# Performance work log

Measured on AMD Instinct MI355X. Metric: run time of the kernel, lower is better.

Reference implementation:

```python
import jax, jax.numpy as jnp
import numpy as np

EPS_S = 1e-06
EPS_SUM = 1e-08
EPS_LOG = 1e-08


def gram_eigh_svd(h_flat):
    """h_flat: (B, N, k) float32 -> (S: (B,k) desc, Vh: (B,k,k)).
    SVD of h_flat via eigendecomposition of the k x k gram matrix."""
    G = jnp.einsum('bnk,bnm->bkm', h_flat, h_flat)  # (B, k, k)
    evals, evecs = jnp.linalg.eigh(G)               # ascending eigenvalues
    S = jnp.sqrt(jnp.clip(evals, 0.0, None))[:, ::-1]          # descending
    Vh = jnp.swapaxes(evecs[:, :, ::-1], -2, -1)                # rows = right singular vectors
    return S, Vh


def extract_features(S, Vh):
    """(B,k), (B,k,k) -> (B, 2k+2)."""
    S_safe = jnp.clip(S, EPS_S, None)
    s_norm = S_safe / (jnp.sum(S_safe, axis=-1, keepdims=True) + EPS_SUM)
    vh_diag = jnp.diagonal(Vh, axis1=-2, axis2=-1)                       # (B, k)
    vh_offdiag = jnp.clip(
        jnp.sum(Vh * Vh, axis=(-2, -1)) - jnp.sum(vh_diag * vh_diag, axis=-1),
        0.0, None)[:, None]                                              # (B, 1)
    s_ent = -jnp.sum(s_norm * jnp.log(jnp.clip(s_norm, EPS_LOG, None)),
                     axis=-1, keepdims=True)                             # (B, 1)
    out = jnp.concatenate([s_norm, vh_diag, vh_offdiag, s_ent], axis=-1)
    return jnp.where(jnp.isfinite(out), out, jnp.zeros_like(out))


def setup_inputs() -> dict:
    key = jax.random.key(0)
    k1, k2 = jax.random.split(key)
    B, C, H, W = 64, 512, 64, 64
    k = 24
    x = jax.random.normal(k1, (B, C, H, W), dtype=jnp.float32)
    w_proj = jax.random.normal(k2, (k, C), dtype=jnp.float32) * (1.0 / np.sqrt(C))
    ema_s = jnp.ones((k,), dtype=jnp.float32)
    return {"x": x, "w_proj": w_proj, "ema_s": ema_s}


def reference(x, w_proj, ema_s):
    B, C, H, W = x.shape
    k = w_proj.shape[0]
    # 1x1 conv == per-pixel matmul; go straight to (B, H*W, k)
    h_flat = jnp.einsum('bchw,kc->bhwk', x, w_proj).reshape(B, H * W, k)
    # torch path runs eigh under no_grad / fp32
    S, Vh = gram_eigh_svd(jax.lax.stop_gradient(h_flat.astype(jnp.float32)))
    S = jnp.clip(S, EPS_S, None)
    S = jnp.where(jnp.isfinite(S), S, jnp.ones_like(S))
    Vh = jnp.where(jnp.isfinite(Vh), Vh, jnp.zeros_like(Vh))
    features = extract_features(S, Vh)
    novelty = S - ema_s[None, :]
    return (S, Vh, features, novelty)
```

## Files before the change

### kernel.cpp

```cpp
#include <hip/hip_runtime.h>
#include <math.h>


#define N24 24
#define ZS 25

__global__ __launch_bounds__(256) void proj_gram_kernel(
    const float* __restrict__ x, const float* __restrict__ w,
    double* __restrict__ partial)
{
    const int b   = blockIdx.x >> 2;
    const int q   = blockIdx.x & 3;
    const int tid = threadIdx.x;
    const int n0  = (q << 10) | (tid << 2);
    __shared__ __align__(16) float smem[24 * 512];
    float* wl = smem;
    for (int i2 = tid; i2 < 24 * 512; i2 += 256) wl[i2] = w[i2];
    __syncthreads();

    const float* xb = x + ((size_t)b << 21) + n0;
    float h[4][24];
#pragma unroll
    for (int j = 0; j < 4; ++j)
#pragma unroll
        for (int k = 0; k < 24; ++k) h[j][k] = 0.f;

    float4 cA[8];
#pragma unroll
    for (int t = 0; t < 8; ++t)
        cA[t] = *reinterpret_cast<const float4*>(xb + ((size_t)t << 12));

    for (int c = 0; c < 512; c += 8) {
        float4 cB[8];
        if (c + 8 < 512) {
#pragma unroll
            for (int t = 0; t < 8; ++t)
                cB[t] = *reinterpret_cast<const float4*>(xb + ((size_t)(c + 8 + t) << 12));
        }
#pragma unroll
        for (int sub = 0; sub < 2; ++sub) {
            const float4 a0 = cA[sub * 4 + 0];
            const float4 a1 = cA[sub * 4 + 1];
            const float4 a2 = cA[sub * 4 + 2];
            const float4 a3 = cA[sub * 4 + 3];
            const int cc = c + sub * 4;
#pragma unroll
            for (int k = 0; k < 24; ++k) {
                const float4 wv = *reinterpret_cast<const float4*>(&wl[k * 512 + cc]);
                h[0][k] += wv.x * a0.x + wv.y * a1.x + wv.z * a2.x + wv.w * a3.x;
                h[1][k] += wv.x * a0.y + wv.y * a1.y + wv.z * a2.y + wv.w * a3.y;
                h[2][k] += wv.x * a0.z + wv.y * a1.z + wv.z * a2.z + wv.w * a3.z;
                h[3][k] += wv.x * a0.w + wv.y * a1.w + wv.z * a2.w + wv.w * a3.w;
            }
        }
#pragma unroll
        for (int t = 0; t < 8; ++t) cA[t] = cB[t];
    }
    __syncthreads();

    float* hl = smem;
    const int s_own = tid >> 6, l64 = tid & 63;
    for (int s2 = 0; s2 < 4; ++s2) {
        if (s_own == s2) {
#pragma unroll
            for (int j = 0; j < 4; ++j)
#pragma unroll
                for (int k = 0; k < 24; ++k)
                    hl[((l64 << 2) + j) * 24 + k] = h[j][k];
        }
        __syncthreads();
        for (int p = tid; p < 300; p += 256) {
            int k = 0, pp = p;
            while (pp >= 24 - k) { pp -= 24 - k; ++k; }
            int m = k + pp;
            double acc = 0.0;
            for (int i2 = 0; i2 < 256; ++i2)
                acc += (double)hl[i2 * 24 + k] * (double)hl[i2 * 24 + m];
            partial[((size_t)(b * 16 + (q << 2) + s2)) * 300 + p] = acc;
        }
        __syncthreads();
    }
}

__global__ __launch_bounds__(320) void gram_reduce_kernel(
    const double* __restrict__ partial, float* __restrict__ G)
{
    const int b = blockIdx.x;
    const int p = threadIdx.x;
    if (p >= 300) return;
    int k = 0, pp = p;
    while (pp >= 24 - k) { pp -= 24 - k; ++k; }
    int m = k + pp;
    double acc = 0.0;
    for (int t = 0; t < 16; ++t)
        acc += partial[((size_t)(b * 16 + t)) * 300 + p];
    float v = (float)acc;
    G[b * 576 + k * 24 + m] = v;
    G[b * 576 + m * 24 + k] = v;
}

__device__ __forceinline__ float rlf(float v, int l) {
    return __int_as_float(__builtin_amdgcn_readlane(__float_as_int(v), l));
}

__device__ __forceinline__ float lapy2f(float xx, float yy) {
#pragma clang fp contract(off)
    float xa = fabsf(xx), ya = fabsf(yy);
    float w = fmaxf(xa, ya), z = fminf(xa, ya);
    float q = z / w;
    float res = w * sqrtf(1.f + q * q);
    return (z == 0.f) ? w : res;
}

__device__ __forceinline__ void slartg_(float f, float g, float& c, float& s, float& r) {
#pragma clang fp contract(off)
    float f1 = fabsf(f), g1 = fabsf(g);
    const float rtmin_ = 0x1p-63f;
    const float rtmax_ = 1.8446743e+19f;
    bool inr = (f1 > rtmin_) && (f1 < rtmax_) && (g1 > rtmin_) && (g1 < rtmax_);
    if (__builtin_expect(!inr && f != 0.f && g != 0.f, 0)) {
        float u = fminf(3.4028235e+38f, fmaxf(0x1p-126f, fmaxf(f1, g1)));
        float fs = f / u, gs = g / u;
        float d = sqrtf(fs * fs + gs * gs);
        float p = 1.f / d;
        c = fabsf(fs) * p;
        s = gs * copysignf(p, f);
        r = copysignf(d, f) * u;
    } else {
        float d = sqrtf(f * f + g * g);
        float p = 1.f / d;
        float cN = f1 * p;
        float sN = g * copysignf(p, f);
        float rN = copysignf(d, f);
        bool gz = (g == 0.f), fz = (f == 0.f);
        c = gz ? 1.f : (fz ? 0.f : cN);
        s = gz ? 0.f : (fz ? copysignf(1.f, g) : sN);
        r = gz ? f   : (fz ? g1 : rN);
    }
}

__device__ __forceinline__ void slaev2_(float a, float b, float cc,
                                        float& rt1, float& rt2, float& cs1, float& sn1) {
#pragma clang fp contract(off)
    float sm = a + cc, df = a - cc, adf = fabsf(df);
    float tb = b + b, ab = fabsf(tb);
    float acmx, acmn;
    if (fabsf(a) > fabsf(cc)) { acmx = a; acmn = cc; } else { acmx = cc; acmn = a; }
    float rt;
    if (adf > ab)      { float q = ab / adf; rt = adf * sqrtf(1.f + q * q); }
    else if (adf < ab) { float q = adf / ab; rt = ab * sqrtf(1.f + q * q); }
    else               rt = ab * sqrtf(2.f);
    int sgn1;
    if (sm < 0.f)      { rt1 = 0.5f * (sm - rt); sgn1 = -1; rt2 = (acmx / rt1) * acmn - (b / rt1) * b; }
    else if (sm > 0.f) { rt1 = 0.5f * (sm + rt); sgn1 =  1; rt2 = (acmx / rt1) * acmn - (b / rt1) * b; }
    else               { rt1 = 0.5f * rt; rt2 = -0.5f * rt; sgn1 = 1; }
    float cs; int sgn2;
    if (df >= 0.f) { cs = df + rt; sgn2 = 1; } else { cs = df - rt; sgn2 = -1; }
    float acs = fabsf(cs);
    if (acs > ab) { float ct = -tb / cs; sn1 = 1.f / sqrtf(1.f + ct * ct); cs1 = ct * sn1; }
    else {
        if (ab == 0.f) { cs1 = 1.f; sn1 = 0.f; }
        else { float tn = -cs / tb; cs1 = 1.f / sqrtf(1.f + tn * tn); sn1 = tn * cs1; }
    }
    if (sgn1 == sgn2) { float tn = cs1; cs1 = -sn1; sn1 = tn; }
}

#define RD(j)   rlf(dr, (j) - 1)
#define RE(j)   rlf(er, (j) - 1)
#define WD(j,v) { float _v = (v); int _j = (j) - 1; dr = (lane == _j) ? _v : dr; }
#define WE(j,v) { float _v = (v); int _j = (j) - 1; er = (lane == _j) ? _v : er; }

__global__ __launch_bounds__(64) void eigh_feat_kernel(
    const float* __restrict__ G, const float* __restrict__ ema,
    float* __restrict__ out)
{
#pragma clang fp contract(off)
    const int b = blockIdx.x;
    const int lane = threadIdx.x;
    const int n = N24;

    __shared__ float A[N24 * N24];
    __shared__ float Zl[N24 * ZS];
    __shared__ float dl[N24 + 1], el[N24 + 1], tau[N24 + 1];
    __shared__ float hv[N24], hw[N24];
    __shared__ float Sarr[N24], snorm[N24];

    for (int idx = lane; idx < n * n; idx += 64) A[idx] = G[(size_t)b * n * n + idx];
    __syncthreads();

    for (int i = 0; i < n - 1; ++i) {
        const int mlen = n - 1 - i;
        float alpha = A[(i + 1) + N24 * i];
        float ss = 0.f;
        for (int r = i + 2; r < n; ++r) { float t = A[r + N24 * i]; ss += t * t; }
        float xnorm = sqrtf(ss);
        if (xnorm == 0.f) {
            if (lane == 0) { tau[i + 1] = 0.f; el[i + 1] = alpha; dl[i + 1] = A[i + N24 * i]; }
            __syncthreads();
            continue;
        }
        float beta = -copysignf(lapy2f(alpha, xnorm), alpha);
        float taui = (beta - alpha) / beta;
        float scal = 1.f / (alpha - beta);
        if (lane == 0) { tau[i + 1] = taui; el[i + 1] = beta; }
        __syncthreads();
        if (lane >= i + 2 && lane < n) A[lane + N24 * i] *= scal;
        __syncthreads();
        if (lane < mlen) hv[lane] = (lane == 0) ? 1.f : A[(i + 1 + lane) + N24 * i];
        __syncthreads();
        if (lane < mlen) {
            float acc = 0.f;
            int gr = i + 1 + lane;
            for (int c2 = 0; c2 < mlen; ++c2) {
                int gc = i + 1 + c2;
                float av = (gr >= gc) ? A[gr + N24 * gc] : A[gc + N24 * gr];
                acc += av * hv[c2];
            }
            hw[lane] = taui * acc;
        }
        __syncthreads();
        float dot = 0.f;
        for (int r2 = 0; r2 < mlen; ++r2) dot += hw[r2] * hv[r2];
        float alpha2 = -0.5f * taui * dot;
        __syncthreads();
        if (lane < mlen) hw[lane] += alpha2 * hv[lane];
        __syncthreads();
        if (lane < mlen) {
            for (int c2 = 0; c2 <= lane; ++c2)
                A[(i + 1 + lane) + N24 * (i + 1 + c2)] -= hv[lane] * hw[c2] + hw[lane] * hv[c2];
        }
        __syncthreads();
        if (lane == 0) dl[i + 1] = A[i + N24 * i];
        __syncthreads();
    }
    if (lane == 0) dl[n] = A[(n - 1) + N24 * (n - 1)];
    __syncthreads();

    for (int idx = lane; idx < N24 * ZS; idx += 64) Zl[idx] = 0.f;
    __syncthreads();
    if (lane < n) Zl[lane + ZS * lane] = 1.f;
    __syncthreads();

    float dr = (lane < 24) ? dl[lane + 1] : 0.f;
    float er = (lane < 23) ? el[lane + 1] : 0.f;
    float wcr = 0.f, wsr = 0.f;

    {
        const float eps_    = 0x1p-24f;
        const float eps2_   = 0x1p-48f;
        const float safmin_ = 0x1p-126f;
        const float ssfmax_ = 3.0744573e+18f;
        const float ssfmin_ = 0x1p-15f;
        const int nmaxit = n * 30;
        int jtot = 0, l1 = 1;
        int l = 0, lsv = 0, lend = 0, lendsv = 0, mb = 0, iscale = 0;
        float anorm = 0.f, p = 0.f, g = 0.f, r_ = 0.f, c_ = 0.f, s_ = 0.f, f_ = 0.f, b_ = 0.f;
        float rt1 = 0.f, rt2 = 0.f, cc = 0.f, sn = 0.f;
        int m_ = 0, i_ = 0, j_ = 0;

L10:
        if (l1 > n) goto L160;
        if (l1 > 1) WE(l1 - 1, 0.f);
        {
            float dnx = __shfl_down(dr, 1, 64);
            float ae = fabsf(er);
            bool inr = (lane >= l1 - 1) && (lane <= n - 2);
            bool t0 = inr && (ae == 0.f);
            bool t1 = inr && (ae <= (sqrtf(fabsf(dr)) * sqrtf(fabsf(dnx))) * eps_);
            unsigned long long msk0 = __ballot(t0);
            unsigned long long mskc = msk0 | __ballot(t1);
            if (mskc) {
                int bit = __builtin_ctzll(mskc);
                m_ = bit + 1;
                bool wasz = (msk0 >> bit) & 1ull;
                if (!wasz) WE(m_, 0.f);
            } else m_ = n;
        }
        l = l1; lsv = l; lend = m_; lendsv = lend; l1 = m_ + 1;
        if (lend == l) goto L10;

        {
            bool ind = (lane >= l - 1) && (lane <= lend - 1);
            bool ine = (lane >= l - 1) && (lane <= lend - 2);
            float v = fmaxf(ind ? fabsf(dr) : 0.f, ine ? fabsf(er) : 0.f);
            for (int off = 32; off; off >>= 1) v = fmaxf(v, __shfl_xor(v, off, 64));
            anorm = v;
        }
        iscale = 0;
        if (anorm == 0.f) goto L10;
        if (anorm > ssfmax_) {
            iscale = 1;
            float mul = ssfmax_ / anorm;
            if (lane + 1 >= l && lane + 1 <= lend) dr *= mul;
            if (lane + 1 >= l && lane + 1 <= lend - 1) er *= mul;
        } else if (anorm < ssfmin_) {
            iscale = 2;
            float mul = ssfmin_ / anorm;
            if (lane + 1 >= l && lane + 1 <= lend) dr *= mul;
            if (lane + 1 >= l && lane + 1 <= lend - 1) er *= mul;
        }
        if (fabsf(RD(lend)) < fabsf(RD(l))) { lend = lsv; l = lendsv; }

        if (lend > l) {
L40:
            if (l != lend) {
                float dnx = __shfl_down(dr, 1, 64);
                bool inr = (lane >= l - 1) && (lane <= lend - 2);
                bool t = inr && (er * er <= (eps2_ * fabsf(dr)) * fabsf(dnx) + safmin_);
                unsigned long long msk = __ballot(t);
                m_ = msk ? (__builtin_ctzll(msk) + 1) : lend;
            } else m_ = lend;
            if (m_ < lend) WE(m_, 0.f);
            mb = m_;
            p = RD(l);
            if (mb == l) goto L80;
            if (mb == l + 1) {
                slaev2_(RD(l), RE(l), RD(l + 1), rt1, rt2, cc, sn);
                if (lane < n) {
                    float z1 = Zl[lane + ZS * l];
                    float z0 = Zl[lane + ZS * (l - 1)];
                    Zl[lane + ZS * l]       = cc * z1 - sn * z0;
                    Zl[lane + ZS * (l - 1)] = sn * z1 + cc * z0;
                }
                WD(l, rt1); WD(l + 1, rt2); WE(l, 0.f);
                l = l + 2;
                if (l <= lend) goto L40;
                goto L140;
            }
            if (jtot == nmaxit) goto L140;
            jtot = jtot + 1;
            {
                float dmb = RD(mb);
                g = (RD(l + 1) - p) / (2.f * RE(l));
                r_ = lapy2f(g, 1.f);
                g = dmb - p + (RE(l) / (g + copysignf(r_, g)));
                s_ = 1.f; c_ = 1.f; p = 0.f;
                float dcar = dmb;
                for (i_ = mb - 1; i_ >= l; --i_) {
                    float ei = RE(i_);
                    float di = RD(i_);
                    f_ = s_ * ei;
                    b_ = c_ * ei;
                    slartg_(g, f_, c_, s_, r_);
                    er = ((i_ != mb - 1) && (lane == i_)) ? r_ : er;
                    g = dcar - p;
                    r_ = (di - g) * s_ + 2.f * c_ * b_;
                    p = s_ * r_;
                    dr = (lane == i_) ? (g + p) : dr;
                    g = c_ * r_ - b_;
                    bool w3 = (lane == i_ - 1);
                    wcr = w3 ? c_ : wcr;
                    wsr = w3 ? -s_ : wsr;
                    dcar = di;
                }
                if (lane < n) {
                    float carry = Zl[lane + ZS * (mb - 1)];
                    for (j_ = mb - 1; j_ >= l; --j_) {
                        float cj = rlf(wcr, j_ - 1), sj = rlf(wsr, j_ - 1);
                        float prev = Zl[lane + ZS * (j_ - 1)];
                        Zl[lane + ZS * j_] = cj * carry - sj * prev;
                        carry = sj * carry + cj * prev;
                    }
                    Zl[lane + ZS * (l - 1)] = carry;
                }
                WD(l, dcar - p);
                WE(l, g);
            }
            goto L40;
L80:
            WD(l, p);
            l = l + 1;
            if (l <= lend) goto L40;
            goto L140;
        } else {
L90:
            if (l != lend) {
                float epu = __shfl_up(er, 1, 64);
                float dup = __shfl_up(dr, 1, 64);
                bool inr = (lane >= lend) && (lane <= l - 1);
                bool t = inr && (epu * epu <= (eps2_ * fabsf(dr)) * fabsf(dup) + safmin_);
                unsigned long long msk = __ballot(t);
                if (msk) {
                    m_ = 63 - __builtin_clzll(msk) + 1;
                } else m_ = lend;
            } else m_ = lend;
            if (m_ > lend) WE(m_ - 1, 0.f);
            mb = m_;
            p = RD(l);
            if (mb == l) goto L130;
            if (mb == l - 1) {
                slaev2_(RD(l - 1), RE(l - 1), RD(l), rt1, rt2, cc, sn);
                if (lane < n) {
                    float z1 = Zl[lane + ZS * (l - 1)];
                    float z0 = Zl[lane + ZS * (l - 2)];
                    Zl[lane + ZS * (l - 1)] = cc * z1 - sn * z0;
                    Zl[lane + ZS * (l - 2)] = sn * z1 + cc * z0;
                }
                WD(l - 1, rt1); WD(l, rt2); WE(l - 1, 0.f);
                l = l - 2;
                if (l >= lend) goto L90;
                goto L140;
            }
            if (jtot == nmaxit) goto L140;
            jtot = jtot + 1;
            {
                float dmb = RD(mb);
                g = (RD(l - 1) - p) / (2.f * RE(l - 1));
                r_ = lapy2f(g, 1.f);
                g = dmb - p + (RE(l - 1) / (g + copysignf(r_, g)));
                s_ = 1.f; c_ = 1.f; p = 0.f;
                float dcar = dmb;
                for (i_ = mb; i_ <= l - 1; ++i_) {
                    float ei = RE(i_);
                    float dnx = RD(i_ + 1);
                    f_ = s_ * ei;
                    b_ = c_ * ei;
                    slartg_(g, f_, c_, s_, r_);
                    er = ((i_ != mb) && (lane == i_ - 2)) ? r_ : er;
                    g = dcar - p;
                    r_ = (dnx - g) * s_ + 2.f * c_ * b_;
                    p = s_ * r_;
                    dr = (lane == i_ - 1) ? (g + p) : dr;
                    g = c_ * r_ - b_;
                    bool w3 = (lane == i_ - 1);
                    wcr = w3 ? c_ : wcr;
                    wsr = w3 ? s_ : wsr;
                    dcar = dnx;
                }
                if (lane < n) {
                    float carryPrev = Zl[lane + ZS * (mb - 1)];
                    for (j_ = mb; j_ <= l - 1; ++j_) {
                        float cj = rlf(wcr, j_ - 1), sj = rlf(wsr, j_ - 1);
                        float t = Zl[lane + ZS * j_];
                        Zl[lane + ZS * (j_ - 1)] = sj * t + cj * carryPrev;
                        carryPrev = cj * t - sj * carryPrev;
                    }
                    Zl[lane + ZS * (l - 1)] = carryPrev;
                }
                WD(l, dcar - p);
                WE(l - 1, g);
            }
            goto L90;
L130:
            WD(l, p);
            l = l - 1;
            if (l >= lend) goto L90;
            goto L140;
        }
L140:
        if (iscale == 1) {
            float mul = anorm / ssfmax_;
            if (lane + 1 >= lsv && lane + 1 <= lendsv) dr *= mul;
            if (lane + 1 >= lsv && lane + 1 <= lendsv - 1) er *= mul;
        } else if (iscale == 2) {
            float mul = anorm / ssfmin_;
            if (lane + 1 >= lsv && lane + 1 <= lendsv) dr *= mul;
            if (lane + 1 >= lsv && lane + 1 <= lendsv - 1) er *= mul;
        }
        if (jtot < nmaxit) goto L10;
        goto L160;

L160:
        for (int ii = 2; ii <= n; ++ii) {
            int ia = ii - 1;
            float val = (lane >= ii - 2 && lane <= n - 1) ? dr : __builtin_inff();
            int idx = lane + 1;
            for (int off = 32; off; off >>= 1) {
                float v2 = __shfl_xor(val, off, 64);
                int   i2 = __shfl_xor(idx, off, 64);
                bool take = (v2 < val) || ((v2 == val) && (i2 < idx));
                val = take ? v2 : val;
                idx = take ? i2 : idx;
            }
            int ka = idx;
            float pp = val;
            if (ka != ia) {
                float dia = RD(ia);
                WD(ka, dia);
                WD(ia, pp);
                if (lane < n) {
                    float t = Zl[lane + ZS * (ia - 1)];
                    Zl[lane + ZS * (ia - 1)] = Zl[lane + ZS * (ka - 1)];
                    Zl[lane + ZS * (ka - 1)] = t;
                }
            }
        }
    }

    if (lane < 24) dl[lane + 1] = dr;
    __syncthreads();

    for (int i = n - 2; i >= 0; --i) {
        float taui = tau[i + 1];
        if (taui != 0.f && lane < n) {
            int j = lane;
            float w_ = Zl[(i + 1) + ZS * j];
            for (int r = i + 2; r < n; ++r) w_ += A[r + N24 * i] * Zl[r + ZS * j];
            Zl[(i + 1) + ZS * j] -= taui * w_;
            for (int r = i + 2; r < n; ++r) Zl[r + ZS * j] -= taui * (A[r + N24 * i] * w_);
        }
        __syncthreads();
    }

    const int S_OFF = 0, VH_OFF = 1536, F_OFF = 38400, NOV_OFF = 41600;
    if (lane < n) {
        float ev = dl[n - lane];
        float s0 = sqrtf(fmaxf(ev, 0.f));
        s0 = fmaxf(s0, 1e-6f);
        if (!isfinite(s0)) s0 = 1.f;
        Sarr[lane] = s0;
    }
    __syncthreads();
    if (lane < n) {
        out[S_OFF + b * 24 + lane] = Sarr[lane];
        out[NOV_OFF + b * 24 + lane] = Sarr[lane] - ema[lane];
    }
    for (int idx = lane; idx < 576; idx += 64) {
        int j = idx / 24, i2 = idx % 24;
        float vv = Zl[i2 + ZS * (23 - j)];
        if (!isfinite(vv)) vv = 0.f;
        out[VH_OFF + b * 576 + idx] = vv;
    }
    float sum_ = 0.f;
    for (int j2 = 0; j2 < n; ++j2) sum_ += Sarr[j2];
    float denom = sum_ + 1e-8f;
    if (lane < n) snorm[lane] = Sarr[lane] / denom;
    __syncthreads();
    float ent = 0.f;
    for (int j2 = 0; j2 < n; ++j2) {
        float sn2 = snorm[j2];
        ent -= sn2 * logf(fmaxf(sn2, 1e-8f));
    }
    float sumsq = 0.f, diagsq = 0.f;
    for (int j2 = 0; j2 < n; ++j2)
        for (int i2 = 0; i2 < n; ++i2) { float z = Zl[i2 + ZS * j2]; sumsq += z * z; }
    for (int j2 = 0; j2 < n; ++j2) { float dv = Zl[j2 + ZS * (23 - j2)]; diagsq += dv * dv; }
    float offd = fmaxf(sumsq - diagsq, 0.f);
    if (lane < n) {
        float v0 = snorm[lane]; if (!isfinite(v0)) v0 = 0.f;
        out[F_OFF + b * 50 + lane] = v0;
        float dv = Zl[lane + ZS * (23 - lane)]; if (!isfinite(dv)) dv = 0.f;
        out[F_OFF + b * 50 + 24 + lane] = dv;
    }
    if (lane == 0) {
        if (!isfinite(offd)) offd = 0.f;
        if (!isfinite(ent)) ent = 0.f;
        out[F_OFF + b * 50 + 48] = offd;
        out[F_OFF + b * 50 + 49] = ent;
    }
}

extern "C" void kernel_launch(void* const* d_in, const int* in_sizes, int n_in,
                              void* d_out, int out_size, void* d_ws, size_t ws_size,
                              hipStream_t stream)
{
    const float* x   = (const float*)d_in[0];
    const float* w   = (const float*)d_in[1];
    const float* ema = (const float*)d_in[2];
    float* out = (float*)d_out;

    double* partial = (double*)d_ws;
    float* G = (float*)((char*)d_ws + (size_t)1024 * 300 * sizeof(double));

    hipLaunchKernelGGL(proj_gram_kernel, dim3(256), dim3(256), 0, stream, x, w, partial);
    hipLaunchKernelGGL(gram_reduce_kernel, dim3(64), dim3(320), 0, stream, partial, G);
    hipLaunchKernelGGL(eigh_feat_kernel, dim3(64), dim3(64), 0, stream, G, ema, out);
}
```

Before: 507.7 us.

## Double projection grid to 512 blocks and split eigh into three kernels

```diff
diff --git a/kernel.cpp b/kernel.cpp
--- a/kernel.cpp
+++ b/kernel.cpp
@@ -4,53 +4,52 @@
 
 #define N24 24
 #define ZS 25
+#define HS 25
 
 __global__ __launch_bounds__(256) void proj_gram_kernel(
     const float* __restrict__ x, const float* __restrict__ w,
     double* __restrict__ partial)
 {
-    const int b   = blockIdx.x >> 2;
-    const int q   = blockIdx.x & 3;
+    const int b   = blockIdx.x >> 3;
+    const int q8  = blockIdx.x & 7;
     const int tid = threadIdx.x;
-    const int n0  = (q << 10) | (tid << 2);
-    __shared__ __align__(16) float smem[24 * 512];
+    const int n0  = (q8 << 9) | (tid << 1);
+    __shared__ __align__(16) float smem[512 * HS];
     float* wl = smem;
     for (int i2 = tid; i2 < 24 * 512; i2 += 256) wl[i2] = w[i2];
     __syncthreads();
 
     const float* xb = x + ((size_t)b << 21) + n0;
-    float h[4][24];
-#pragma unroll
-    for (int j = 0; j < 4; ++j)
+    float h[2][24];
+#pragma unroll
+    for (int j = 0; j < 2; ++j)
 #pragma unroll
         for (int k = 0; k < 24; ++k) h[j][k] = 0.f;
 
-    float4 cA[8];
+    float2 cA[8];
 #pragma unroll
     for (int t = 0; t < 8; ++t)
-        cA[t] = *reinterpret_cast<const float4*>(xb + ((size_t)t << 12));
+        cA[t] = *reinterpret_cast<const float2*>(xb + ((size_t)t << 12));
 
     for (int c = 0; c < 512; c += 8) {
-        float4 cB[8];
+        float2 cB[8];
         if (c + 8 < 512) {
 #pragma unroll
             for (int t = 0; t < 8; ++t)
-                cB[t] = *reinterpret_cast<const float4*>(xb + ((size_t)(c + 8 + t) << 12));
+                cB[t] = *reinterpret_cast<const float2*>(xb + ((size_t)(c + 8 + t) << 12));
         }
 #pragma unroll
         for (int sub = 0; sub < 2; ++sub) {
-            const float4 a0 = cA[sub * 4 + 0];
-            const float4 a1 = cA[sub * 4 + 1];
-            const float4 a2 = cA[sub * 4 + 2];
-            const float4 a3 = cA[sub * 4 + 3];
+            const float2 a0 = cA[sub * 4 + 0];
+            const float2 a1 = cA[sub * 4 + 1];
+            const float2 a2 = cA[sub * 4 + 2];
+            const float2 a3 = cA[sub * 4 + 3];
             const int cc = c + sub * 4;
 #pragma unroll
             for (int k = 0; k < 24; ++k) {
                 const float4 wv = *reinterpret_cast<const float4*>(&wl[k * 512 + cc]);
                 h[0][k] += wv.x * a0.x + wv.y * a1.x + wv.z * a2.x + wv.w * a3.x;
                 h[1][k] += wv.x * a0.y + wv.y * a1.y + wv.z * a2.y + wv.w * a3.y;
-                h[2][k] += wv.x * a0.z + wv.y * a1.z + wv.z * a2.z + wv.w * a3.z;
-                h[3][k] += wv.x * a0.w + wv.y * a1.w + wv.z * a2.w + wv.w * a3.w;
             }
         }
 #pragma unroll
@@ -59,26 +58,24 @@
     __syncthreads();
 
     float* hl = smem;
-    const int s_own = tid >> 6, l64 = tid & 63;
-    for (int s2 = 0; s2 < 4; ++s2) {
-        if (s_own == s2) {
-#pragma unroll
-            for (int j = 0; j < 4; ++j)
-#pragma unroll
-                for (int k = 0; k < 24; ++k)
-                    hl[((l64 << 2) + j) * 24 + k] = h[j][k];
-        }
-        __syncthreads();
+#pragma unroll
+    for (int j = 0; j < 2; ++j)
+#pragma unroll
+        for (int k = 0; k < 24; ++k)
+            hl[((tid << 1) + j) * HS + k] = h[j][k];
+    __syncthreads();
+
+    for (int s2 = 0; s2 < 2; ++s2) {
+        const float* hb = hl + s2 * 256 * HS;
         for (int p = tid; p < 300; p += 256) {
             int k = 0, pp = p;
             while (pp >= 24 - k) { pp -= 24 - k; ++k; }
             int m = k + pp;
             double acc = 0.0;
             for (int i2 = 0; i2 < 256; ++i2)
-                acc += (double)hl[i2 * 24 + k] * (double)hl[i2 * 24 + m];
-            partial[((size_t)(b * 16 + (q << 2) + s2)) * 300 + p] = acc;
-        }
-        __syncthreads();
+                acc += (double)hb[i2 * HS + k] * (double)hb[i2 * HS + m];
+            partial[((size_t)(b * 16 + (q8 << 1) + s2)) * 300 + p] = acc;
+        }
     }
 }
 
@@ -170,9 +167,9 @@
 #define WD(j,v) { float _v = (v); int _j = (j) - 1; dr = (lane == _j) ? _v : dr; }
 #define WE(j,v) { float _v = (v); int _j = (j) - 1; er = (lane == _j) ? _v : er; }
 
-__global__ __launch_bounds__(64) void eigh_feat_kernel(
-    const float* __restrict__ G, const float* __restrict__ ema,
-    float* __restrict__ out)
+__global__ __launch_bounds__(64) void eigh_tridiag_kernel(
+    const float* __restrict__ G, float* __restrict__ Aout,
+    float* __restrict__ taug, float* __restrict__ deg)
 {
 #pragma clang fp contract(off)
     const int b = blockIdx.x;
@@ -180,10 +177,8 @@
     const int n = N24;
 
     __shared__ float A[N24 * N24];
-    __shared__ float Zl[N24 * ZS];
     __shared__ float dl[N24 + 1], el[N24 + 1], tau[N24 + 1];
     __shared__ float hv[N24], hw[N24];
-    __shared__ float Sarr[N24], snorm[N24];
 
     for (int idx = lane; idx < n * n; idx += 64) A[idx] = G[(size_t)b * n * n + idx];
     __syncthreads();
@@ -236,13 +231,30 @@
     if (lane == 0) dl[n] = A[(n - 1) + N24 * (n - 1)];
     __syncthreads();
 
+    for (int idx = lane; idx < n * n; idx += 64) Aout[b * 576 + idx] = A[idx];
+    if (lane < 24) deg[b * 64 + lane] = dl[lane + 1];
+    if (lane < 23) deg[b * 64 + 32 + lane] = el[lane + 1];
+    if (lane >= 1 && lane < 24) taug[b * 32 + lane] = tau[lane];
+}
+
+__global__ __launch_bounds__(64) void eigh_steqr_kernel(
+    const float* __restrict__ deg, float* __restrict__ Zout,
+    float* __restrict__ dsort)
+{
+#pragma clang fp contract(off)
+    const int b = blockIdx.x;
+    const int lane = threadIdx.x;
+    const int n = N24;
+
+    __shared__ float Zl[N24 * ZS];
+
     for (int idx = lane; idx < N24 * ZS; idx += 64) Zl[idx] = 0.f;
     __syncthreads();
     if (lane < n) Zl[lane + ZS * lane] = 1.f;
     __syncthreads();
 
-    float dr = (lane < 24) ? dl[lane + 1] : 0.f;
-    float er = (lane < 23) ? el[lane + 1] : 0.f;
+    float dr = (lane < 24) ? deg[b * 64 + lane] : 0.f;
+    float er = (lane < 23) ? deg[b * 64 + 32 + lane] : 0.f;
     float wcr = 0.f, wsr = 0.f;
 
     {
@@ -486,8 +498,31 @@
             }
         }
     }
-
-    if (lane < 24) dl[lane + 1] = dr;
+    __syncthreads();
+
+    for (int idx = lane; idx < N24 * ZS; idx += 64) Zout[b * (N24 * ZS) + idx] = Zl[idx];
+    if (lane < 24) dsort[b * 32 + lane] = dr;
+}
+
+__global__ __launch_bounds__(64) void eigh_back_feat_kernel(
+    const float* __restrict__ Ain, const float* __restrict__ taug,
+    const float* __restrict__ Zin, const float* __restrict__ dsort,
+    const float* __restrict__ ema, float* __restrict__ out)
+{
+#pragma clang fp contract(off)
+    const int b = blockIdx.x;
+    const int lane = threadIdx.x;
+    const int n = N24;
+
+    __shared__ float A[N24 * N24];
+    __shared__ float Zl[N24 * ZS];
+    __shared__ float dl[N24 + 1], tau[N24 + 1];
+    __shared__ float Sarr[N24], snorm[N24];
+
+    for (int idx = lane; idx < n * n; idx += 64) A[idx] = Ain[b * 576 + idx];
+    for (int idx = lane; idx < N24 * ZS; idx += 64) Zl[idx] = Zin[b * (N24 * ZS) + idx];
+    if (lane >= 1 && lane < 24) tau[lane] = taug[b * 32 + lane];
+    if (lane < 24) dl[lane + 1] = dsort[b * 32 + lane];
     __syncthreads();
 
     for (int i = n - 2; i >= 0; --i) {
@@ -559,10 +594,18 @@
     const float* ema = (const float*)d_in[2];
     float* out = (float*)d_out;
 
-    double* partial = (double*)d_ws;
-    float* G = (float*)((char*)d_ws + (size_t)1024 * 300 * sizeof(double));
-
-    hipLaunchKernelGGL(proj_gram_kernel, dim3(256), dim3(256), 0, stream, x, w, partial);
+    char* wsb = (char*)d_ws;
+    double* partial = (double*)(wsb + 0);
+    float*  G       = (float*)(wsb + 2457600);
+    float*  Aout    = (float*)(wsb + 2605056);
+    float*  taug    = (float*)(wsb + 2752512);
+    float*  deg     = (float*)(wsb + 2760704);
+    float*  Zout    = (float*)(wsb + 2777088);
+    float*  dsort   = (float*)(wsb + 2930688);
+
+    hipLaunchKernelGGL(proj_gram_kernel, dim3(512), dim3(256), 0, stream, x, w, partial);
     hipLaunchKernelGGL(gram_reduce_kernel, dim3(64), dim3(320), 0, stream, partial, G);
-    hipLaunchKernelGGL(eigh_feat_kernel, dim3(64), dim3(64), 0, stream, G, ema, out);
-}
+    hipLaunchKernelGGL(eigh_tridiag_kernel, dim3(64), dim3(64), 0, stream, G, Aout, taug, deg);
+    hipLaunchKernelGGL(eigh_steqr_kernel, dim3(64), dim3(64), 0, stream, deg, Zout, dsort);
+    hipLaunchKernelGGL(eigh_back_feat_kernel, dim3(64), dim3(64), 0, stream, Aout, taug, Zout, dsort, ema, out);
+}
```

After: 511.3 us. No clear change (+0.7%).
